# Kernel tuning notes

Hardware: AMD Instinct MI355X
Metric: run time of the kernel (lower is better)

The kernel has to match this reference:

```python
import jax, jax.numpy as jnp
import numpy as np

B, D, R = 8192, 4096, 64
REG_W, REG_C = 0.01, 0.05


def setup_inputs() -> dict:
    key = jax.random.key(0)
    ks = jax.random.split(key, 7)
    return {
        "X": jax.random.normal(ks[0], (B, D), dtype=jnp.float32),
        "U1": jax.random.normal(ks[1], (1, D, R), dtype=jnp.float32),
        "U2": jax.random.normal(ks[2], (2, D, R), dtype=jnp.float32),
        "U3": jax.random.normal(ks[3], (3, D, R), dtype=jnp.float32),
        "C": jax.random.normal(ks[4], (3,), dtype=jnp.float32),
        "beta": jax.random.normal(ks[5], (1,), dtype=jnp.float32),
        "C_sin": jax.random.normal(ks[6], (1,), dtype=jnp.float32),
    }


def reference(X, U1, U2, U3, C, beta, C_sin):
    # term_j(x) = sum_r prod_{i<=j} <x, U_j[i, :, r]>
    result = jnp.broadcast_to(beta[0], (X.shape[0],))
    reg_loss_w = jnp.float32(0.0)
    for j, U in enumerate((U1, U2, U3)):
        dots = jnp.einsum("bd,odr->obr", X, U)      # [order, B, R]
        term = jnp.prod(dots, axis=0).sum(axis=1)   # [B]
        result = result + C[j] * term
        reg_loss_w = reg_loss_w + REG_W * (jnp.abs(U).sum() / U.size)
    sine_term = C_sin[0] * jnp.sin(X).sum(axis=1)
    result = result + sine_term
    reg_loss_c = REG_C * (jnp.abs(C).sum() + jnp.abs(C_sin).sum())
    total_reg = reg_loss_w + reg_loss_c
    return result, total_reg
```

## Files before the change

### kernel.cpp

```cpp
#include <hip/hip_runtime.h>
#include <hip/hip_bf16.h>

typedef float f32x4 __attribute__((ext_vector_type(4)));
typedef short s16x8 __attribute__((ext_vector_type(8)));

#define D_DIM 4096
#define NT 24
#define NSLAB_H 64
#define BM 64
#define DSTRIDE 392
#define POOL_BYTES (64 * DSTRIDE * 4)
#define PART_OFF (4u << 20)
#define SINW_OFF (28u << 20)

__device__ __forceinline__ unsigned short f2bf(float f) {
    unsigned u = __float_as_uint(f);
    u += 0x7fffu + ((u >> 16) & 1u);
    return (unsigned short)(u >> 16);
}

__global__ __launch_bounds__(64) void reg_init_kernel(const float* __restrict__ C,
                                                      const float* __restrict__ Csin,
                                                      float* __restrict__ reg_out) {
    if (threadIdx.x == 0)
        reg_out[0] = 0.05f * (fabsf(C[0]) + fabsf(C[1]) + fabsf(C[2]) + fabsf(Csin[0]));
}

__global__ __launch_bounds__(64) void build_w_kernel(const float* __restrict__ U1,
                                                     const float* __restrict__ U2,
                                                     const float* __restrict__ U3,
                                                     unsigned short* __restrict__ W,
                                                     float* __restrict__ reg_out) {
    const int ks = blockIdx.x / NT;
    const int ct = blockIdx.x % NT;
    const int l  = threadIdx.x;
    const int n  = ct * 16 + (l & 15);
    const int kb = ks * 32 + ((l >> 4) << 3);

    const float* src;
    float scale;
    if (n < 64)       { src = U1 + n;                  scale = 0.01f / 262144.f; }
    else if (n < 128) { src = U2 + (n - 64);           scale = 0.01f / 524288.f; }
    else if (n < 192) { src = U2 + 262144 + (n - 128); scale = 0.01f / 524288.f; }
    else if (n < 256) { src = U3 + (n - 192);          scale = 0.01f / 786432.f; }
    else if (n < 320) { src = U3 + 262144 + (n - 256); scale = 0.01f / 786432.f; }
    else              { src = U3 + 524288 + (n - 320); scale = 0.01f / 786432.f; }

    unsigned short h[8];
    float sabs = 0.f;
#pragma unroll
    for (int j = 0; j < 8; ++j) {
        float u = src[(size_t)(kb + j) * 64];
        sabs += fabsf(u);
        h[j] = f2bf(u);
    }
    uint4 pk;
    pk.x = (unsigned)h[0] | ((unsigned)h[1] << 16);
    pk.y = (unsigned)h[2] | ((unsigned)h[3] << 16);
    pk.z = (unsigned)h[4] | ((unsigned)h[5] << 16);
    pk.w = (unsigned)h[6] | ((unsigned)h[7] << 16);
    *(uint4*)(W + ((size_t)blockIdx.x * 64 + l) * 8) = pk;

    sabs *= scale;
#pragma unroll
    for (int off = 32; off >= 1; off >>= 1)
        sabs += __shfl_xor(sabs, off, 64);
    if (l == 0) atomicAdd(reg_out, sabs);
}

__global__ __launch_bounds__(1024) void poly_main_kernel(const float* __restrict__ X,
                                                         const unsigned short* __restrict__ W,
                                                         float* __restrict__ part,
                                                         float* __restrict__ sinws) {
    __shared__ __align__(16) char pool[POOL_BYTES];

    const int t    = threadIdx.x;
    const int lane = t & 63;
    const int wv   = t >> 6;
    const int kg   = wv >> 3;
    const int cg   = wv & 7;
    const int ct0  = cg * 3;
    const int rb   = blockIdx.x >> 1;
    const int kh   = blockIdx.x & 1;
    const int row0 = rb * BM;

    const int p    = t >> 9;
    const int srow = (t >> 3) & 63;
    const int k4   = (t & 7) << 2;
    const float* xp = X + (size_t)(row0 + srow) * D_DIM + kh * 2048 + k4;
    const int awfrag = (srow >> 4) * 1024
                     + (((((k4 >> 3) & 3) << 4) | (srow & 15)) * 16) + ((k4 & 7) << 1);

    const s16x8* __restrict__ Wh = (const s16x8*)W + (size_t)kh * NSLAB_H * NT * 64;

    f32x4 acc[4][3];
#pragma unroll
    for (int r = 0; r < 4; ++r)
#pragma unroll
        for (int c = 0; c < 3; ++c) acc[r][c] = (f32x4){0.f, 0.f, 0.f, 0.f};
    float sinacc = 0.f;
    f32x4 xw{}, xa{}, xb{};

    {
        f32x4 x0 = *(const f32x4*)(xp + (size_t)p * 32);
        sinacc += __sinf(x0.x) + __sinf(x0.y) + __sinf(x0.z) + __sinf(x0.w);
        short4 h;
        h.x = (short)f2bf(x0.x); h.y = (short)f2bf(x0.y);
        h.z = (short)f2bf(x0.z); h.w = (short)f2bf(x0.w);
        *(short4*)(pool + p * 4096 + awfrag) = h;
        xw = *(const f32x4*)(xp + (size_t)(2 + p) * 32);
        xa = *(const f32x4*)(xp + (size_t)(4 + p) * 32);
        xb = *(const f32x4*)(xp + (size_t)(6 + p) * 32);
    }
    s16x8 bA0 = Wh[((size_t)kg * NT + ct0 + 0) * 64 + lane];
    s16x8 bA1 = Wh[((size_t)kg * NT + ct0 + 1) * 64 + lane];
    s16x8 bA2 = Wh[((size_t)kg * NT + ct0 + 2) * 64 + lane];
    s16x8 bB0{}, bB1{}, bB2{};
    asm volatile("s_waitcnt lgkmcnt(0)" ::: "memory");
    __builtin_amdgcn_s_barrier();
    __builtin_amdgcn_sched_barrier(0);

#define BODY(d_, U0, U1, U2, P0, P1, P2, XW)                                    \
    {                                                                           \
        const int d__ = (d_);                                                   \
        const int sw_ = 2 * d__ + 2 + p;                                        \
        if (sw_ < NSLAB_H) {                                                    \
            sinacc += __sinf(XW.x) + __sinf(XW.y)                               \
                    + __sinf(XW.z) + __sinf(XW.w);                              \
            short4 h_;                                                          \
            h_.x = (short)f2bf(XW.x); h_.y = (short)f2bf(XW.y);                 \
            h_.z = (short)f2bf(XW.z); h_.w = (short)f2bf(XW.w);                 \
            *(short4*)(pool + (sw_ & 3) * 4096 + awfrag) = h_;                  \
        }                                                                       \
        int sl_ = 2 * d__ + 8 + p; if (sl_ > NSLAB_H - 1) sl_ = NSLAB_H - 1;    \
        XW = *(const f32x4*)(xp + (size_t)sl_ * 32);                            \
        int sp_ = 2 * d__ + 2 + kg; if (sp_ > NSLAB_H - 1) sp_ = NSLAB_H - 1;   \
        P0 = Wh[((size_t)sp_ * NT + ct0 + 0) * 64 + lane];                      \
        P1 = Wh[((size_t)sp_ * NT + ct0 + 1) * 64 + lane];                      \
        P2 = Wh[((size_t)sp_ * NT + ct0 + 2) * 64 + lane];                      \
        const int ab_ = ((2 * d__ + kg) & 3) * 4096;                            \
        s16x8 af0_ = *(const s16x8*)(pool + ab_ + 0 * 1024 + lane * 16);        \
        s16x8 af1_ = *(const s16x8*)(pool + ab_ + 1 * 1024 + lane * 16);        \
        s16x8 af2_ = *(const s16x8*)(pool + ab_ + 2 * 1024 + lane * 16);        \
        s16x8 af3_ = *(const s16x8*)(pool + ab_ + 3 * 1024 + lane * 16);        \
        asm volatile("s_waitcnt lgkmcnt(0)" ::: "memory");                      \
        __builtin_amdgcn_sched_barrier(0);                                      \
        __builtin_amdgcn_s_setprio(1);                                          \
        acc[0][0] = __builtin_amdgcn_mfma_f32_16x16x32_bf16(af0_, U0, acc[0][0], 0, 0, 0); \
        acc[0][1] = __builtin_amdgcn_mfma_f32_16x16x32_bf16(af0_, U1, acc[0][1], 0, 0, 0); \
        acc[0][2] = __builtin_amdgcn_mfma_f32_16x16x32_bf16(af0_, U2, acc[0][2], 0, 0, 0); \
        acc[1][0] = __builtin_amdgcn_mfma_f32_16x16x32_bf16(af1_, U0, acc[1][0], 0, 0, 0); \
        acc[1][1] = __builtin_amdgcn_mfma_f32_16x16x32_bf16(af1_, U1, acc[1][1], 0, 0, 0); \
        acc[1][2] = __builtin_amdgcn_mfma_f32_16x16x32_bf16(af1_, U2, acc[1][2], 0, 0, 0); \
        acc[2][0] = __builtin_amdgcn_mfma_f32_16x16x32_bf16(af2_, U0, acc[2][0], 0, 0, 0); \
        acc[2][1] = __builtin_amdgcn_mfma_f32_16x16x32_bf16(af2_, U1, acc[2][1], 0, 0, 0); \
        acc[2][2] = __builtin_amdgcn_mfma_f32_16x16x32_bf16(af2_, U2, acc[2][2], 0, 0, 0); \
        acc[3][0] = __builtin_amdgcn_mfma_f32_16x16x32_bf16(af3_, U0, acc[3][0], 0, 0, 0); \
        acc[3][1] = __builtin_amdgcn_mfma_f32_16x16x32_bf16(af3_, U1, acc[3][1], 0, 0, 0); \
        acc[3][2] = __builtin_amdgcn_mfma_f32_16x16x32_bf16(af3_, U2, acc[3][2], 0, 0, 0); \
        __builtin_amdgcn_s_setprio(0);                                          \
        __builtin_amdgcn_s_barrier();                                           \
        __builtin_amdgcn_sched_barrier(0);                                      \
    }

    for (int e = 0; e < 5; ++e) {
        const int d0 = 6 * e;
        BODY(d0 + 0, bA0, bA1, bA2, bB0, bB1, bB2, xw);
        BODY(d0 + 1, bB0, bB1, bB2, bA0, bA1, bA2, xa);
        BODY(d0 + 2, bA0, bA1, bA2, bB0, bB1, bB2, xb);
        BODY(d0 + 3, bB0, bB1, bB2, bA0, bA1, bA2, xw);
        BODY(d0 + 4, bA0, bA1, bA2, bB0, bB1, bB2, xa);
        BODY(d0 + 5, bB0, bB1, bB2, bA0, bA1, bA2, xb);
    }
    BODY(30, bA0, bA1, bA2, bB0, bB1, bB2, xw);
    BODY(31, bB0, bB1, bB2, bA0, bA1, bA2, xa);
#undef BODY

    float* Dm = (float*)pool;
    const int lr4 = (lane >> 4) << 2;
    const int lc  = lane & 15;

    if (kg == 0) {
#pragma unroll
        for (int r = 0; r < 4; ++r)
#pragma unroll
            for (int c = 0; c < 3; ++c) {
                const int col = (ct0 + c) * 16 + lc;
#pragma unroll
                for (int i = 0; i < 4; ++i)
                    Dm[(r * 16 + lr4 + i) * DSTRIDE + col] = acc[r][c][i];
            }
    }
    __syncthreads();
    if (kg == 1) {
#pragma unroll
        for (int r = 0; r < 4; ++r)
#pragma unroll
            for (int c = 0; c < 3; ++c) {
                const int col = (ct0 + c) * 16 + lc;
#pragma unroll
                for (int i = 0; i < 4; ++i)
                    Dm[(r * 16 + lr4 + i) * DSTRIDE + col] += acc[r][c][i];
            }
    }
    sinacc += __shfl_xor(sinacc, 1);
    sinacc += __shfl_xor(sinacc, 2);
    sinacc += __shfl_xor(sinacc, 4);
    if ((t & 7) == 0)
        sinws[(size_t)(kh * 2 + p) * 8192 + row0 + srow] = sinacc;
    __syncthreads();

    float* pb = part + ((size_t)kh * 128 + rb) * (BM * 384);
    const int prow = t >> 4;
    const int pc0  = (t & 15) * 24;
#pragma unroll
    for (int v = 0; v < 6; ++v)
        *(f32x4*)(pb + (size_t)prow * 384 + pc0 + v * 4) =
            *(const f32x4*)(Dm + prow * DSTRIDE + pc0 + v * 4);
}

__global__ __launch_bounds__(512) void combine_kernel(const float* __restrict__ part,
                                                      const float* __restrict__ sinws,
                                                      const float* __restrict__ C,
                                                      const float* __restrict__ beta,
                                                      const float* __restrict__ Csin,
                                                      float* __restrict__ out) {
    const int t   = threadIdx.x;
    const int row = blockIdx.x * 32 + (t >> 4);
    const int cc  = t & 15;
    const int rb  = row >> 6;
    const int lr  = row & 63;
    const float* p0 = part + (size_t)rb * (64 * 384) + (size_t)lr * 384;
    const float* p1 = p0 + (size_t)128 * (64 * 384);

    float t1 = 0.f, t2 = 0.f, t3 = 0.f;
#pragma unroll
    for (int rr = 0; rr < 64; rr += 16) {
        const int c = rr + cc;
        const float d1 = p0[c]       + p1[c];
        const float a2 = p0[64 + c]  + p1[64 + c];
        const float b2 = p0[128 + c] + p1[128 + c];
        const float a3 = p0[192 + c] + p1[192 + c];
        const float b3 = p0[256 + c] + p1[256 + c];
        const float c3 = p0[320 + c] + p1[320 + c];
        t1 += d1;
        t2 += a2 * b2;
        t3 += a3 * b3 * c3;
    }
#pragma unroll
    for (int off = 1; off < 16; off <<= 1) {
        t1 += __shfl_xor(t1, off, 16);
        t2 += __shfl_xor(t2, off, 16);
        t3 += __shfl_xor(t3, off, 16);
    }
    if (cc == 0) {
        const float s = sinws[row] + sinws[8192 + row]
                      + sinws[2 * 8192 + row] + sinws[3 * 8192 + row];
        out[row] = beta[0] + C[0] * t1 + C[1] * t2 + C[2] * t3 + Csin[0] * s;
    }
}

extern "C" void kernel_launch(void* const* d_in, const int* in_sizes, int n_in,
                              void* d_out, int out_size, void* d_ws, size_t ws_size,
                              hipStream_t stream) {
    const float* X   = (const float*)d_in[0];
    const float* U1  = (const float*)d_in[1];
    const float* U2  = (const float*)d_in[2];
    const float* U3  = (const float*)d_in[3];
    const float* Cc  = (const float*)d_in[4];
    const float* bet = (const float*)d_in[5];
    const float* Cs  = (const float*)d_in[6];
    float* out = (float*)d_out;

    unsigned short* W = (unsigned short*)d_ws;
    float* part  = (float*)((char*)d_ws + PART_OFF);
    float* sinws = (float*)((char*)d_ws + SINW_OFF);

    reg_init_kernel<<<1, 64, 0, stream>>>(Cc, Cs, out + 8192);
    build_w_kernel<<<128 * NT, 64, 0, stream>>>(U1, U2, U3, W, out + 8192);
    poly_main_kernel<<<256, 1024, 0, stream>>>(X, W, part, sinws);
    combine_kernel<<<256, 512, 0, stream>>>(part, sinws, Cc, bet, Cs, out);
}
```

Measured before the change: 99.93 us.

## Halve row tile to 32 and drop in-block K-split reduction through LDS

The main kernel moves from 256 blocks of 1024 threads with 64-row tiles and two in-block K-groups to 512 blocks of 512 threads with 32-row tiles. Each wave now covers both K-slabs itself, with a 2x3 accumulator layout and six B fragments per step. The LDS reduction between K-groups and the staged copy-out are gone: accumulators are written straight to global partials, and LDS shrinks to a double buffer. This aims for more blocks per CU and less epilogue sync, at the cost of reading W twice as often per output row and issuing uncoalesced scalar stores for the partials.

```diff
diff --git a/kernel.cpp b/kernel.cpp
--- a/kernel.cpp
+++ b/kernel.cpp
@@ -6,12 +6,10 @@
 
 #define D_DIM 4096
 #define NT 24
-#define NSLAB_H 64
-#define BM 64
-#define DSTRIDE 392
-#define POOL_BYTES (64 * DSTRIDE * 4)
+#define NBODY 32
+#define BM 32
 #define PART_OFF (4u << 20)
-#define SINW_OFF (28u << 20)
+#define SINW_OFF ((4u << 20) + 25165824u)
 
 __device__ __forceinline__ unsigned short f2bf(float f) {
     unsigned u = __float_as_uint(f);
@@ -68,96 +66,94 @@
     if (l == 0) atomicAdd(reg_out, sabs);
 }
 
-__global__ __launch_bounds__(1024) void poly_main_kernel(const float* __restrict__ X,
-                                                         const unsigned short* __restrict__ W,
-                                                         float* __restrict__ part,
-                                                         float* __restrict__ sinws) {
-    __shared__ __align__(16) char pool[POOL_BYTES];
+__global__ __launch_bounds__(512, 4) void poly_main_kernel(const float* __restrict__ X,
+                                                           const unsigned short* __restrict__ W,
+                                                           float* __restrict__ part,
+                                                           float* __restrict__ sinws) {
+    __shared__ __align__(16) char pool[8192 + 128];
 
     const int t    = threadIdx.x;
     const int lane = t & 63;
     const int wv   = t >> 6;
-    const int kg   = wv >> 3;
-    const int cg   = wv & 7;
-    const int ct0  = cg * 3;
+    const int ct0  = wv * 3;
     const int rb   = blockIdx.x >> 1;
     const int kh   = blockIdx.x & 1;
     const int row0 = rb * BM;
 
-    const int p    = t >> 9;
-    const int srow = (t >> 3) & 63;
-    const int k4   = (t & 7) << 2;
+    const int srow = t >> 4;
+    const int k4   = (t & 15) << 2;
     const float* xp = X + (size_t)(row0 + srow) * D_DIM + kh * 2048 + k4;
-    const int awfrag = (srow >> 4) * 1024
-                     + (((((k4 >> 3) & 3) << 4) | (srow & 15)) * 16) + ((k4 & 7) << 1);
-
-    const s16x8* __restrict__ Wh = (const s16x8*)W + (size_t)kh * NSLAB_H * NT * 64;
-
-    f32x4 acc[4][3];
-#pragma unroll
-    for (int r = 0; r < 4; ++r)
-#pragma unroll
-        for (int c = 0; c < 3; ++c) acc[r][c] = (f32x4){0.f, 0.f, 0.f, 0.f};
+    const int awfrag = (k4 >> 5) * 2048 + (srow >> 4) * 1024
+                     + (((((k4 & 31) >> 3) << 4) | (srow & 15)) * 16) + ((k4 & 7) << 1);
+
+    const s16x8* __restrict__ Wh = (const s16x8*)W + (size_t)kh * 64 * NT * 64;
+
+    f32x4 acc00{}, acc01{}, acc02{}, acc10{}, acc11{}, acc12{};
     float sinacc = 0.f;
     f32x4 xw{}, xa{}, xb{};
 
     {
-        f32x4 x0 = *(const f32x4*)(xp + (size_t)p * 32);
+        f32x4 x0 = *(const f32x4*)xp;
         sinacc += __sinf(x0.x) + __sinf(x0.y) + __sinf(x0.z) + __sinf(x0.w);
         short4 h;
         h.x = (short)f2bf(x0.x); h.y = (short)f2bf(x0.y);
         h.z = (short)f2bf(x0.z); h.w = (short)f2bf(x0.w);
-        *(short4*)(pool + p * 4096 + awfrag) = h;
-        xw = *(const f32x4*)(xp + (size_t)(2 + p) * 32);
-        xa = *(const f32x4*)(xp + (size_t)(4 + p) * 32);
-        xb = *(const f32x4*)(xp + (size_t)(6 + p) * 32);
-    }
-    s16x8 bA0 = Wh[((size_t)kg * NT + ct0 + 0) * 64 + lane];
-    s16x8 bA1 = Wh[((size_t)kg * NT + ct0 + 1) * 64 + lane];
-    s16x8 bA2 = Wh[((size_t)kg * NT + ct0 + 2) * 64 + lane];
-    s16x8 bB0{}, bB1{}, bB2{};
+        *(short4*)(pool + awfrag) = h;
+        xw = *(const f32x4*)(xp + 64);
+        xa = *(const f32x4*)(xp + 128);
+        xb = *(const f32x4*)(xp + 192);
+    }
+    s16x8 bA0 = Wh[((size_t)0 * NT + ct0 + 0) * 64 + lane];
+    s16x8 bA1 = Wh[((size_t)0 * NT + ct0 + 1) * 64 + lane];
+    s16x8 bA2 = Wh[((size_t)0 * NT + ct0 + 2) * 64 + lane];
+    s16x8 bA3 = Wh[((size_t)1 * NT + ct0 + 0) * 64 + lane];
+    s16x8 bA4 = Wh[((size_t)1 * NT + ct0 + 1) * 64 + lane];
+    s16x8 bA5 = Wh[((size_t)1 * NT + ct0 + 2) * 64 + lane];
+    s16x8 bB0{}, bB1{}, bB2{}, bB3{}, bB4{}, bB5{};
     asm volatile("s_waitcnt lgkmcnt(0)" ::: "memory");
     __builtin_amdgcn_s_barrier();
     __builtin_amdgcn_sched_barrier(0);
 
-#define BODY(d_, U0, U1, U2, P0, P1, P2, XW)                                    \
+#define BODY(d_, U0, U1, U2, U3, U4, U5, P0, P1, P2, P3, P4, P5, XW)            \
     {                                                                           \
         const int d__ = (d_);                                                   \
-        const int sw_ = 2 * d__ + 2 + p;                                        \
-        if (sw_ < NSLAB_H) {                                                    \
+        if (d__ + 1 < NBODY) {                                                  \
             sinacc += __sinf(XW.x) + __sinf(XW.y)                               \
                     + __sinf(XW.z) + __sinf(XW.w);                              \
             short4 h_;                                                          \
             h_.x = (short)f2bf(XW.x); h_.y = (short)f2bf(XW.y);                 \
             h_.z = (short)f2bf(XW.z); h_.w = (short)f2bf(XW.w);                 \
-            *(short4*)(pool + (sw_ & 3) * 4096 + awfrag) = h_;                  \
+            *(short4*)(pool + ((d__ + 1) & 1) * 4096 + awfrag) = h_;            \
         }                                                                       \
-        int sl_ = 2 * d__ + 8 + p; if (sl_ > NSLAB_H - 1) sl_ = NSLAB_H - 1;    \
-        XW = *(const f32x4*)(xp + (size_t)sl_ * 32);                            \
-        int sp_ = 2 * d__ + 2 + kg; if (sp_ > NSLAB_H - 1) sp_ = NSLAB_H - 1;   \
-        P0 = Wh[((size_t)sp_ * NT + ct0 + 0) * 64 + lane];                      \
-        P1 = Wh[((size_t)sp_ * NT + ct0 + 1) * 64 + lane];                      \
-        P2 = Wh[((size_t)sp_ * NT + ct0 + 2) * 64 + lane];                      \
-        const int ab_ = ((2 * d__ + kg) & 3) * 4096;                            \
-        s16x8 af0_ = *(const s16x8*)(pool + ab_ + 0 * 1024 + lane * 16);        \
-        s16x8 af1_ = *(const s16x8*)(pool + ab_ + 1 * 1024 + lane * 16);        \
-        s16x8 af2_ = *(const s16x8*)(pool + ab_ + 2 * 1024 + lane * 16);        \
-        s16x8 af3_ = *(const s16x8*)(pool + ab_ + 3 * 1024 + lane * 16);        \
+        int sl_ = d__ + 4; if (sl_ > NBODY - 1) sl_ = NBODY - 1;                \
+        XW = *(const f32x4*)(xp + (size_t)sl_ * 64);                            \
+        int sp_ = d__ + 1; if (sp_ > NBODY - 1) sp_ = NBODY - 1;                \
+        P0 = Wh[((size_t)(2 * sp_ + 0) * NT + ct0 + 0) * 64 + lane];            \
+        P1 = Wh[((size_t)(2 * sp_ + 0) * NT + ct0 + 1) * 64 + lane];            \
+        P2 = Wh[((size_t)(2 * sp_ + 0) * NT + ct0 + 2) * 64 + lane];            \
+        P3 = Wh[((size_t)(2 * sp_ + 1) * NT + ct0 + 0) * 64 + lane];            \
+        P4 = Wh[((size_t)(2 * sp_ + 1) * NT + ct0 + 1) * 64 + lane];            \
+        P5 = Wh[((size_t)(2 * sp_ + 1) * NT + ct0 + 2) * 64 + lane];            \
+        const int ab_ = (d__ & 1) * 4096;                                       \
+        s16x8 a00_ = *(const s16x8*)(pool + ab_ +        lane * 16);            \
+        s16x8 a10_ = *(const s16x8*)(pool + ab_ + 1024 + lane * 16);            \
+        s16x8 a01_ = *(const s16x8*)(pool + ab_ + 2048 + lane * 16);            \
+        s16x8 a11_ = *(const s16x8*)(pool + ab_ + 3072 + lane * 16);            \
         asm volatile("s_waitcnt lgkmcnt(0)" ::: "memory");                      \
         __builtin_amdgcn_sched_barrier(0);                                      \
         __builtin_amdgcn_s_setprio(1);                                          \
-        acc[0][0] = __builtin_amdgcn_mfma_f32_16x16x32_bf16(af0_, U0, acc[0][0], 0, 0, 0); \
-        acc[0][1] = __builtin_amdgcn_mfma_f32_16x16x32_bf16(af0_, U1, acc[0][1], 0, 0, 0); \
-        acc[0][2] = __builtin_amdgcn_mfma_f32_16x16x32_bf16(af0_, U2, acc[0][2], 0, 0, 0); \
-        acc[1][0] = __builtin_amdgcn_mfma_f32_16x16x32_bf16(af1_, U0, acc[1][0], 0, 0, 0); \
-        acc[1][1] = __builtin_amdgcn_mfma_f32_16x16x32_bf16(af1_, U1, acc[1][1], 0, 0, 0); \
-        acc[1][2] = __builtin_amdgcn_mfma_f32_16x16x32_bf16(af1_, U2, acc[1][2], 0, 0, 0); \
-        acc[2][0] = __builtin_amdgcn_mfma_f32_16x16x32_bf16(af2_, U0, acc[2][0], 0, 0, 0); \
-        acc[2][1] = __builtin_amdgcn_mfma_f32_16x16x32_bf16(af2_, U1, acc[2][1], 0, 0, 0); \
-        acc[2][2] = __builtin_amdgcn_mfma_f32_16x16x32_bf16(af2_, U2, acc[2][2], 0, 0, 0); \
-        acc[3][0] = __builtin_amdgcn_mfma_f32_16x16x32_bf16(af3_, U0, acc[3][0], 0, 0, 0); \
-        acc[3][1] = __builtin_amdgcn_mfma_f32_16x16x32_bf16(af3_, U1, acc[3][1], 0, 0, 0); \
-        acc[3][2] = __builtin_amdgcn_mfma_f32_16x16x32_bf16(af3_, U2, acc[3][2], 0, 0, 0); \
+        acc00 = __builtin_amdgcn_mfma_f32_16x16x32_bf16(a00_, U0, acc00, 0, 0, 0); \
+        acc01 = __builtin_amdgcn_mfma_f32_16x16x32_bf16(a00_, U1, acc01, 0, 0, 0); \
+        acc02 = __builtin_amdgcn_mfma_f32_16x16x32_bf16(a00_, U2, acc02, 0, 0, 0); \
+        acc10 = __builtin_amdgcn_mfma_f32_16x16x32_bf16(a10_, U0, acc10, 0, 0, 0); \
+        acc11 = __builtin_amdgcn_mfma_f32_16x16x32_bf16(a10_, U1, acc11, 0, 0, 0); \
+        acc12 = __builtin_amdgcn_mfma_f32_16x16x32_bf16(a10_, U2, acc12, 0, 0, 0); \
+        acc00 = __builtin_amdgcn_mfma_f32_16x16x32_bf16(a01_, U3, acc00, 0, 0, 0); \
+        acc01 = __builtin_amdgcn_mfma_f32_16x16x32_bf16(a01_, U4, acc01, 0, 0, 0); \
+        acc02 = __builtin_amdgcn_mfma_f32_16x16x32_bf16(a01_, U5, acc02, 0, 0, 0); \
+        acc10 = __builtin_amdgcn_mfma_f32_16x16x32_bf16(a11_, U3, acc10, 0, 0, 0); \
+        acc11 = __builtin_amdgcn_mfma_f32_16x16x32_bf16(a11_, U4, acc11, 0, 0, 0); \
+        acc12 = __builtin_amdgcn_mfma_f32_16x16x32_bf16(a11_, U5, acc12, 0, 0, 0); \
         __builtin_amdgcn_s_setprio(0);                                          \
         __builtin_amdgcn_s_barrier();                                           \
         __builtin_amdgcn_sched_barrier(0);                                      \
@@ -165,58 +161,37 @@
 
     for (int e = 0; e < 5; ++e) {
         const int d0 = 6 * e;
-        BODY(d0 + 0, bA0, bA1, bA2, bB0, bB1, bB2, xw);
-        BODY(d0 + 1, bB0, bB1, bB2, bA0, bA1, bA2, xa);
-        BODY(d0 + 2, bA0, bA1, bA2, bB0, bB1, bB2, xb);
-        BODY(d0 + 3, bB0, bB1, bB2, bA0, bA1, bA2, xw);
-        BODY(d0 + 4, bA0, bA1, bA2, bB0, bB1, bB2, xa);
-        BODY(d0 + 5, bB0, bB1, bB2, bA0, bA1, bA2, xb);
-    }
-    BODY(30, bA0, bA1, bA2, bB0, bB1, bB2, xw);
-    BODY(31, bB0, bB1, bB2, bA0, bA1, bA2, xa);
+        BODY(d0 + 0, bA0, bA1, bA2, bA3, bA4, bA5, bB0, bB1, bB2, bB3, bB4, bB5, xw);
+        BODY(d0 + 1, bB0, bB1, bB2, bB3, bB4, bB5, bA0, bA1, bA2, bA3, bA4, bA5, xa);
+        BODY(d0 + 2, bA0, bA1, bA2, bA3, bA4, bA5, bB0, bB1, bB2, bB3, bB4, bB5, xb);
+        BODY(d0 + 3, bB0, bB1, bB2, bB3, bB4, bB5, bA0, bA1, bA2, bA3, bA4, bA5, xw);
+        BODY(d0 + 4, bA0, bA1, bA2, bA3, bA4, bA5, bB0, bB1, bB2, bB3, bB4, bB5, xa);
+        BODY(d0 + 5, bB0, bB1, bB2, bB3, bB4, bB5, bA0, bA1, bA2, bA3, bA4, bA5, xb);
+    }
+    BODY(30, bA0, bA1, bA2, bA3, bA4, bA5, bB0, bB1, bB2, bB3, bB4, bB5, xw);
+    BODY(31, bB0, bB1, bB2, bB3, bB4, bB5, bA0, bA1, bA2, bA3, bA4, bA5, xa);
 #undef BODY
 
-    float* Dm = (float*)pool;
+    float* pb = part + ((size_t)kh * 256 + rb) * (BM * 384);
     const int lr4 = (lane >> 4) << 2;
     const int lc  = lane & 15;
-
-    if (kg == 0) {
-#pragma unroll
-        for (int r = 0; r < 4; ++r)
-#pragma unroll
-            for (int c = 0; c < 3; ++c) {
-                const int col = (ct0 + c) * 16 + lc;
-#pragma unroll
-                for (int i = 0; i < 4; ++i)
-                    Dm[(r * 16 + lr4 + i) * DSTRIDE + col] = acc[r][c][i];
-            }
-    }
-    __syncthreads();
-    if (kg == 1) {
-#pragma unroll
-        for (int r = 0; r < 4; ++r)
-#pragma unroll
-            for (int c = 0; c < 3; ++c) {
-                const int col = (ct0 + c) * 16 + lc;
-#pragma unroll
-                for (int i = 0; i < 4; ++i)
-                    Dm[(r * 16 + lr4 + i) * DSTRIDE + col] += acc[r][c][i];
-            }
-    }
+    const f32x4 accA[2][3] = {{acc00, acc01, acc02}, {acc10, acc11, acc12}};
+#pragma unroll
+    for (int rf = 0; rf < 2; ++rf)
+#pragma unroll
+        for (int c = 0; c < 3; ++c) {
+            const int col = (ct0 + c) * 16 + lc;
+#pragma unroll
+            for (int i = 0; i < 4; ++i)
+                pb[(size_t)(rf * 16 + lr4 + i) * 384 + col] = accA[rf][c][i];
+        }
+
     sinacc += __shfl_xor(sinacc, 1);
     sinacc += __shfl_xor(sinacc, 2);
     sinacc += __shfl_xor(sinacc, 4);
-    if ((t & 7) == 0)
-        sinws[(size_t)(kh * 2 + p) * 8192 + row0 + srow] = sinacc;
-    __syncthreads();
-
-    float* pb = part + ((size_t)kh * 128 + rb) * (BM * 384);
-    const int prow = t >> 4;
-    const int pc0  = (t & 15) * 24;
-#pragma unroll
-    for (int v = 0; v < 6; ++v)
-        *(f32x4*)(pb + (size_t)prow * 384 + pc0 + v * 4) =
-            *(const f32x4*)(Dm + prow * DSTRIDE + pc0 + v * 4);
+    sinacc += __shfl_xor(sinacc, 8);
+    if ((t & 15) == 0)
+        sinws[(size_t)kh * 8192 + row0 + srow] = sinacc;
 }
 
 __global__ __launch_bounds__(512) void combine_kernel(const float* __restrict__ part,
@@ -228,10 +203,10 @@
     const int t   = threadIdx.x;
     const int row = blockIdx.x * 32 + (t >> 4);
     const int cc  = t & 15;
-    const int rb  = row >> 6;
-    const int lr  = row & 63;
-    const float* p0 = part + (size_t)rb * (64 * 384) + (size_t)lr * 384;
-    const float* p1 = p0 + (size_t)128 * (64 * 384);
+    const int rb  = row >> 5;
+    const int lr  = row & 31;
+    const float* p0 = part + (size_t)rb * (BM * 384) + (size_t)lr * 384;
+    const float* p1 = p0 + (size_t)256 * (BM * 384);
 
     float t1 = 0.f, t2 = 0.f, t3 = 0.f;
 #pragma unroll
@@ -254,8 +229,7 @@
         t3 += __shfl_xor(t3, off, 16);
     }
     if (cc == 0) {
-        const float s = sinws[row] + sinws[8192 + row]
-                      + sinws[2 * 8192 + row] + sinws[3 * 8192 + row];
+        const float s = sinws[row] + sinws[8192 + row];
         out[row] = beta[0] + C[0] * t1 + C[1] * t2 + C[2] * t3 + Csin[0] * s;
     }
 }
@@ -278,6 +252,6 @@
 
     reg_init_kernel<<<1, 64, 0, stream>>>(Cc, Cs, out + 8192);
     build_w_kernel<<<128 * NT, 64, 0, stream>>>(U1, U2, U3, W, out + 8192);
-    poly_main_kernel<<<256, 1024, 0, stream>>>(X, W, part, sinws);
+    poly_main_kernel<<<512, 512, 0, stream>>>(X, W, part, sinws);
     combine_kernel<<<256, 512, 0, stream>>>(part, sinws, Cc, bet, Cs, out);
 }
```

Measured after the change: 103.0 us. 1.03x slower.
